# Optimization experiments

Measured on AMD Instinct MI355X. Metric: run time of the kernel, lower is better.

The kernel has to match this reference:

```python
import jax, jax.numpy as jnp
import numpy as np
from jax import lax

BN_EPS = 1e-5
EYE_EPS = 1e-6
ZIP = 128
TAU = 0.2

def _cov(x):
    # x: [C, N] rows=variables, cols=observations (torch.cov semantics)
    n = x.shape[1]
    xc = x - jnp.mean(x, axis=1, keepdims=True)
    return (xc @ xc.T) / (n - 1)

def setup_inputs() -> dict:
    key = jax.random.key(0)
    ks = jax.random.split(key, 10)
    d = {}
    d["img_feats_f"] = jax.random.normal(ks[0], (1, 128, 480, 640), dtype=jnp.float32)
    d["pcd_feats_f"] = jax.random.normal(ks[1], (22432, 128), dtype=jnp.float32)
    # ConvBlock(128->128, k=3, s=1, p=1) + BatchNorm (eval) + ReLU
    d["conv_w"] = jax.random.normal(ks[2], (128, 128, 3, 3), dtype=jnp.float32) * 0.02
    d["conv_b"] = jnp.zeros((128,), dtype=jnp.float32)
    d["bn_gamma"] = jnp.ones((128,), dtype=jnp.float32)
    d["bn_beta"] = jnp.zeros((128,), dtype=jnp.float32)
    d["bn_mean"] = jnp.zeros((128,), dtype=jnp.float32)
    d["bn_var"] = jnp.ones((128,), dtype=jnp.float32)
    # Linear(128->128) + ReLU
    d["lin_w"] = jax.random.normal(ks[3], (128, 128), dtype=jnp.float32) * 0.02
    d["lin_b"] = jnp.zeros((128,), dtype=jnp.float32)
    return d

def reference(img_feats_f, pcd_feats_f, conv_w, conv_b, bn_gamma, bn_beta, bn_mean, bn_var, lin_w, lin_b):
    B, C, h, w = img_feats_f.shape
    # zip_fea_2d: Conv2d(3x3, pad 1) + BN(eval) + ReLU
    x = lax.conv_general_dilated(img_feats_f, conv_w, (1, 1), ((1, 1), (1, 1)),
                                 dimension_numbers=("NCHW", "OIHW", "NCHW"))
    x = x + conv_b[None, :, None, None]
    x = (x - bn_mean[None, :, None, None]) * (bn_gamma / jnp.sqrt(bn_var + BN_EPS))[None, :, None, None] + bn_beta[None, :, None, None]
    img_zip = jax.nn.relu(x)
    # zip_fea_3d: Linear + ReLU
    pcd_zip = jax.nn.relu(pcd_feats_f @ lin_w.T + lin_b)

    tmp_img_f = img_zip.reshape(ZIP, -1)        # [128, h*w]
    tmp_pcd_f = pcd_zip.T                        # [128, Np]
    cov_img = _cov(tmp_img_f)                    # [128, 128]
    cov_pcd = _cov(tmp_pcd_f)                    # [128, 128]

    eye = jnp.eye(ZIP, dtype=cov_img.dtype) * EYE_EPS
    sc_ip = (cov_img @ jnp.linalg.inv(cov_pcd + eye)) / ZIP
    sc_pi = (cov_pcd @ jnp.linalg.inv(cov_img + eye)) / ZIP
    at_ip = jax.nn.softmax(sc_pi, axis=-1)
    at_pi = jax.nn.softmax(sc_ip, axis=-1)
    tmp_img_fb = (at_ip @ tmp_img_f).reshape(-1, h, w)[None]   # [1,128,h,w]
    tmp_pcd_fb = (at_pi @ tmp_pcd_f).T                          # [Np,128]

    at_ii = jax.nn.softmax((cov_img @ cov_img.T) / ZIP, axis=-1)
    at_pp = jax.nn.softmax((cov_pcd @ cov_pcd.T) / ZIP, axis=-1)
    tmp_img_fa = (at_ii @ tmp_img_f).reshape(-1, h, w)[None]
    tmp_pcd_fa = (at_pp @ tmp_pcd_f).T

    img_out = (tmp_img_fb + tmp_img_fa) / 2 * TAU + img_feats_f * (1 - TAU)
    pcd_out = (tmp_pcd_fb + tmp_pcd_fa) / 2 * TAU + pcd_feats_f * (1 - TAU)
    return (img_out, pcd_out)
```

## Files before the change

kernel.cpp:

```cpp
#include <hip/hip_runtime.h>
#include <math.h>

#define HH 480
#define WW 640
#define HWSZ (HH*WW)
#define NPC 22432
#define IMG_SZ (128*HWSZ)
#define NBI 256
#define NBP 64
#define CHUNK_I 1200
#define CHUNK_P 351

typedef unsigned short u16;
typedef unsigned int u32;
typedef __attribute__((ext_vector_type(8))) short bf16x8;
typedef __attribute__((ext_vector_type(4))) float f32x4;

#define OFF_SUMS_IMG 0
#define OFF_SUMS_PCD 128
#define OFF_BIAS2    256
#define OFF_COV_IMG  512
#define OFF_COV_PCD  16896
#define OFF_INV_IMG  33280
#define OFF_INV_PCD  49664
#define OFF_MT_IMG   66048
#define OFF_MT_PCD   82432
#define OFF_LWT      98816
#define OFF_PSUMS    115200
#define OFF_MB       147968
#define OFF_WT       152064
#define OFF_PSUMS_P  OFF_WT
#define OFF_PART_IMG 299520
#define OFF_PART_PCD 4493824
#define OFF_WB       5542400
#define OFF_TIMG_F   5616128
#define TIMG_PAD_W 642
#define TIMG_PX (482*642)
#define TIMG_PLANE (TIMG_PX*32)
#define WS_NEED_FLOATS 25420544
#define OFF_XB       25420544
#define WS_NEED2_FLOATS 45081344

__device__ inline u32 pack_bf16(float a, float b) {
  u32 ua = __float_as_uint(a), ub = __float_as_uint(b);
  ua += 0x7FFFu + ((ua >> 16) & 1u);
  ub += 0x7FFFu + ((ub >> 16) & 1u);
  return (ua >> 16) | (ub & 0xFFFF0000u);
}
__device__ inline u16 to_bf16(float v) {
  u32 u = __float_as_uint(v); u += 0x7FFFu + ((u >> 16) & 1u);
  return (u16)(u >> 16);
}
__device__ inline float from_bf16(u16 v) {
  return __uint_as_float(((u32)v) << 16);
}
__device__ inline float4 f4_fnma(float4 v, float f, float4 p) {
  return make_float4(v.x - f*p.x, v.y - f*p.y, v.z - f*p.z, v.w - f*p.w);
}
__device__ inline void gload_lds16(const void* g, void* l) {
  __builtin_amdgcn_global_load_lds(
      (const __attribute__((address_space(1))) void*)(g),
      (__attribute__((address_space(3))) void*)(l), 16, 0, 0);
}

__global__ void prep_kernel(const float* __restrict__ conv_w, const float* __restrict__ conv_b,
                            const float* __restrict__ gamma, const float* __restrict__ beta,
                            const float* __restrict__ mean, const float* __restrict__ var,
                            const float* __restrict__ lin_w, float* __restrict__ ws, int big) {
  int tid = blockIdx.x * blockDim.x + threadIdx.x;
  int nth = gridDim.x * blockDim.x;
  for (int oc = tid; oc < 128; oc += nth) {
    float s = gamma[oc] / sqrtf(var[oc] + 1e-5f);
    ws[OFF_BIAS2 + oc] = (conv_b[oc] - mean[oc]) * s + beta[oc];
  }
  if (big) {
    u16* Wf = (u16*)(ws + OFF_WB);
    for (int e = tid; e < 9*128*128; e += nth) {
      int j = e & 7, l = (e >> 3) & 63, ob = (e >> 9) & 7;
      int ci32 = (e >> 12) & 3, tap = e >> 14;
      int oc = ob*16 + (l & 15);
      int ci = ci32*32 + ((l >> 4) & 3)*8 + j;
      float s = gamma[oc] / sqrtf(var[oc] + 1e-5f);
      Wf[e] = to_bf16(conv_w[(oc*128 + ci)*9 + tap] * s);
    }
  } else {
    for (int e = tid; e < 128*9*128; e += nth) {
      int oc = e & 127; int k = (e >> 7) % 9; int ci = e / 1152;
      float s = gamma[oc] / sqrtf(var[oc] + 1e-5f);
      ws[OFF_WT + e] = conv_w[(oc*128 + ci)*9 + k] * s;
    }
  }
  for (int e = tid; e < 128*128; e += nth) {
    int c2 = e & 127; int k = e >> 7;
    ws[OFF_LWT + e] = lin_w[c2*128 + k];
  }
}

__launch_bounds__(256)
__global__ void timg_kernel(const float* __restrict__ img, u16* __restrict__ Timg) {
  __shared__ float xt[64][133];
  const int b = blockIdx.x;
  const int t = threadIdx.x;
  if (b >= 4800) {
    int tid = (b - 4800) * 256 + t;
    if (tid < (642*2 + 480*2) * 16) {
      int px = tid >> 4, u = tid & 15;
      int q = u >> 2, j = u & 3;
      int addr;
      if (px < 642) addr = px;
      else if (px < 1284) addr = 481*642 + (px - 642);
      else if (px < 1764) addr = (px - 1284 + 1) * 642;
      else addr = (px - 1764 + 1) * 642 + 641;
      ((uint4*)Timg)[(size_t)q*(TIMG_PX*4) + (size_t)addr*4 + j] = make_uint4(0u,0u,0u,0u);
    }
    return;
  }
  const int h = b / 10, w0 = (b % 10) * 64;
  const int wq = t & 15, cg = t >> 4;
#pragma unroll
  for (int i = 0; i < 8; ++i) {
    int ci = cg + i*16;
    float4 v = *(const float4*)&img[(size_t)ci*HWSZ + h*WW + w0 + wq*4];
    xt[wq*4+0][ci] = v.x; xt[wq*4+1][ci] = v.y;
    xt[wq*4+2][ci] = v.z; xt[wq*4+3][ci] = v.w;
  }
  __syncthreads();
  const int wp = t >> 2, q = t & 3, c0 = q * 32;
  u32 out[16];
#pragma unroll
  for (int j = 0; j < 16; ++j) {
    float a = xt[wp][c0 + 2*j], bb = xt[wp][c0 + 2*j + 1];
    out[j] = pack_bf16(a, bb);
  }
  uint4 ud[4];
#pragma unroll
  for (int u = 0; u < 4; ++u)
    ud[u] = make_uint4(out[u*4], out[u*4+1], out[u*4+2], out[u*4+3]);
  u16* dst = Timg + (size_t)q*TIMG_PLANE
           + ((size_t)(h+1)*TIMG_PAD_W + (w0 + 1 + wp)) * 32;
  const int key = (1 + wp) & 3;
  uint4* d4 = (uint4*)dst;
  switch (key) {
    case 0: d4[0]=ud[0]; d4[1]=ud[1]; d4[2]=ud[2]; d4[3]=ud[3]; break;
    case 1: d4[0]=ud[1]; d4[1]=ud[0]; d4[2]=ud[3]; d4[3]=ud[2]; break;
    case 2: d4[0]=ud[2]; d4[1]=ud[3]; d4[2]=ud[0]; d4[3]=ud[1]; break;
    default: d4[0]=ud[3]; d4[1]=ud[2]; d4[2]=ud[1]; d4[3]=ud[0]; break;
  }
}

#define REG_ROWS 6
#define REG_COLS 66
#define REG_PX (REG_ROWS*REG_COLS)
#define STAGE_E (REG_PX*4)
__launch_bounds__(256, 2)
__global__ void conv_mfma7_kernel(const u16* __restrict__ Timg,
                                  const u16* __restrict__ Wf,
                                  const float* __restrict__ ws,
                                  float* __restrict__ X,
                                  u16* __restrict__ xb) {
  __shared__ __align__(16) u16 reg_lds[1792 * 8];
  const int b = blockIdx.x;
  const int h0 = (b / 10) * 4;
  const int w0 = (b % 10) * 64;
  const int t = threadIdx.x;
  const int wv = t >> 6, l = t & 63;
  const int n_lane = l & 15, k_lane = l >> 4;
  const int ocg = wv & 1;
  const int rowg = wv >> 1;

  f32x4 acc[4][8];
#pragma unroll
  for (int mt = 0; mt < 4; ++mt)
#pragma unroll
    for (int nt = 0; nt < 8; ++nt) acc[mt][nt] = (f32x4){0.f,0.f,0.f,0.f};

#pragma unroll 1
  for (int qc = 0; qc < 4; ++qc) {
    __syncthreads();
    const u16* plane = Timg + (size_t)qc * TIMG_PLANE;
#pragma unroll
    for (int i = 0; i < 7; ++i) {
      int e = t + i*256;
      int ec = (e < STAGE_E) ? e : (STAGE_E - 1);
      int px = ec >> 2, j = ec & 3;
      int r = px / REG_COLS, c = px - r * REG_COLS;
      const u16* src = plane + ((size_t)(h0 + r) * TIMG_PAD_W + (w0 + c)) * 32 + j*8;
      gload_lds16(src, reg_lds + (size_t)e * 8);
    }
    __syncthreads();
    const u16* wq = Wf + (qc*8 + ocg*4)*512 + l*8;
#pragma unroll 1
    for (int tap = 0; tap < 9; ++tap) {
      const int kh = (tap * 11) >> 5;
      const int kw = tap - kh * 3;
      const int cb = n_lane + kw;
      const int rb = rowg*2 + kh;
      const int uoff = (k_lane ^ (cb & 3)) << 4;
      const u16* wtap = wq + tap * 16384;
      bf16x8 Af[4], Bf[8];
#pragma unroll
      for (int mt = 0; mt < 4; ++mt)
        Af[mt] = *(const bf16x8*)(wtap + mt*512);
#pragma unroll
      for (int nt = 0; nt < 8; ++nt) {
        int px = (rb + (nt >> 2)) * REG_COLS + cb + (nt & 3) * 16;
        Bf[nt] = *(const bf16x8*)((char*)reg_lds + px * 64 + uoff);
      }
#pragma unroll
      for (int mt = 0; mt < 4; ++mt)
#pragma unroll
        for (int nt = 0; nt < 8; ++nt)
          acc[mt][nt] = __builtin_amdgcn_mfma_f32_16x16x32_bf16(Af[mt], Bf[nt], acc[mt][nt], 0, 0, 0);
    }
  }
  const float* bias = ws + OFF_BIAS2;
  if (xb) {
#pragma unroll
    for (int mt = 0; mt < 4; ++mt) {
      f32x4 bv = *(const f32x4*)(bias + ocg*64 + mt*16 + k_lane*4);
#pragma unroll
      for (int nt = 0; nt < 8; ++nt) {
        int row = h0 + rowg*2 + (nt >> 2);
        int col = w0 + (nt & 3)*16 + n_lane;
#pragma unroll
        for (int rr = 0; rr < 4; ++rr) {
          int oc = ocg*64 + mt*16 + k_lane*4 + rr;
          float v = acc[mt][nt][rr] + bv[rr];
          xb[(size_t)oc * HWSZ + row*WW + col] = to_bf16(fmaxf(v, 0.f));
        }
      }
    }
  } else {
#pragma unroll
    for (int mt = 0; mt < 4; ++mt) {
      f32x4 bv = *(const f32x4*)(bias + ocg*64 + mt*16 + k_lane*4);
#pragma unroll
      for (int nt = 0; nt < 8; ++nt) {
        int row = h0 + rowg*2 + (nt >> 2);
        int col = w0 + (nt & 3)*16 + n_lane;
#pragma unroll
        for (int rr = 0; rr < 4; ++rr) {
          int oc = ocg*64 + mt*16 + k_lane*4 + rr;
          float v = acc[mt][nt][rr] + bv[rr];
          X[(size_t)oc * HWSZ + row*WW + col] = fmaxf(v, 0.f);
        }
      }
    }
  }
}

__launch_bounds__(256)
__global__ void conv_kernel(const float* __restrict__ img,
                            const float* __restrict__ ws,
                            float* __restrict__ outX) {
  __shared__ __align__(16) float xs[8][10][20];
  __shared__ __align__(16) float wsm[8][9][64];
  const int b = blockIdx.x;
  const int oc0 = (b & 1) * 64;
  const int sidx = b >> 1;
  const int h0 = (sidx / 40) * 8;
  const int w0 = (sidx % 40) * 16;
  const int t = threadIdx.x;
  const int oc_t = t & 15;
  const int px_t = t >> 4;
  const int ph = px_t >> 1;
  const int pw0 = (px_t & 1) * 8;
  float acc[4][8];
#pragma unroll
  for (int o = 0; o < 4; o++)
#pragma unroll
    for (int m = 0; m < 8; m++) acc[o][m] = 0.f;
  const float* wT = ws + OFF_WT;
  for (int ci0 = 0; ci0 < 128; ci0 += 8) {
    __syncthreads();
    for (int e = t; e < 1440; e += 256) {
      int ci = e / 180; int rem = e - ci*180; int r = rem / 18; int cc2 = rem - r*18;
      int gh = h0 + r - 1, gw = w0 + cc2 - 1;
      float v = 0.f;
      if ((unsigned)gh < (unsigned)HH && (unsigned)gw < (unsigned)WW)
        v = img[(ci0+ci)*HWSZ + gh*WW + gw];
      xs[ci][r][cc2] = v;
    }
    for (int e = t; e < 4608; e += 256) {
      int oc = e & 63; int k = (e >> 6) % 9; int ci = e / 576;
      wsm[ci][k][oc] = wT[((ci0+ci)*9 + k)*128 + oc0 + oc];
    }
    __syncthreads();
#pragma unroll
    for (int ci = 0; ci < 8; ci++) {
#pragma unroll
      for (int kh = 0; kh < 3; kh++) {
        float x10[10];
        float4 xa = *(const float4*)&xs[ci][ph+kh][pw0];
        float4 xb2 = *(const float4*)&xs[ci][ph+kh][pw0+4];
        x10[0]=xa.x; x10[1]=xa.y; x10[2]=xa.z; x10[3]=xa.w;
        x10[4]=xb2.x; x10[5]=xb2.y; x10[6]=xb2.z; x10[7]=xb2.w;
        x10[8]=xs[ci][ph+kh][pw0+8]; x10[9]=xs[ci][ph+kh][pw0+9];
#pragma unroll
        for (int kw = 0; kw < 3; kw++) {
          float4 wv = *(const float4*)&wsm[ci][kh*3+kw][oc_t*4];
#pragma unroll
          for (int m = 0; m < 8; m++) {
            float xv = x10[kw+m];
            acc[0][m] += wv.x*xv; acc[1][m] += wv.y*xv;
            acc[2][m] += wv.z*xv; acc[3][m] += wv.w*xv;
          }
        }
      }
    }
  }
#pragma unroll
  for (int o = 0; o < 4; o++) {
    int oc = oc0 + oc_t*4 + o;
    float bias = ws[OFF_BIAS2 + oc];
    float4 r0, r1;
    r0.x = fmaxf(acc[o][0]+bias, 0.f); r0.y = fmaxf(acc[o][1]+bias, 0.f);
    r0.z = fmaxf(acc[o][2]+bias, 0.f); r0.w = fmaxf(acc[o][3]+bias, 0.f);
    r1.x = fmaxf(acc[o][4]+bias, 0.f); r1.y = fmaxf(acc[o][5]+bias, 0.f);
    r1.z = fmaxf(acc[o][6]+bias, 0.f); r1.w = fmaxf(acc[o][7]+bias, 0.f);
    float* dst = outX + (size_t)oc*HWSZ + (h0+ph)*WW + w0 + pw0;
    *(float4*)dst = r0; *(float4*)(dst+4) = r1;
  }
}

__launch_bounds__(256)
__global__ void linear_kernel(const float* __restrict__ pcd,
                              const float* __restrict__ ws,
                              const float* __restrict__ lin_b,
                              float* __restrict__ Z) {
  __shared__ __align__(16) float Mt[128][132];
  __shared__ __align__(16) float zs[16][132];
  const int b = blockIdx.x, t = threadIdx.x;
  const int n0 = b * 16;
#pragma unroll
  for (int i = 0; i < 16; i++) {
    int idx = t + i*256; int r = idx >> 5; int c4 = (idx & 31)*4;
    *(float4*)&Mt[r][c4] = *(const float4*)&ws[OFF_LWT + r*128 + c4];
  }
#pragma unroll
  for (int i = 0; i < 2; i++) {
    int idx = t + i*256; int r = idx >> 5; int c4 = (idx & 31)*4;
    *(float4*)&zs[r][c4] = *(const float4*)&pcd[(size_t)(n0+r)*128 + c4];
  }
  __syncthreads();
  const int nl = t & 15;
  const int c0 = (t >> 4) * 8;
  float acc[8];
#pragma unroll
  for (int q = 0; q < 8; q++) acc[q] = 0.f;
#pragma unroll 8
  for (int k = 0; k < 128; k++) {
    float z = zs[nl][k];
    float4 wa = *(const float4*)&Mt[k][c0];
    float4 wb = *(const float4*)&Mt[k][c0+4];
    acc[0]+=z*wa.x; acc[1]+=z*wa.y; acc[2]+=z*wa.z; acc[3]+=z*wa.w;
    acc[4]+=z*wb.x; acc[5]+=z*wb.y; acc[6]+=z*wb.z; acc[7]+=z*wb.w;
  }
  float4 ba = *(const float4*)&lin_b[c0];
  float4 bb = *(const float4*)&lin_b[c0+4];
  float4 r0, r1;
  r0.x = fmaxf(acc[0]+ba.x,0.f); r0.y = fmaxf(acc[1]+ba.y,0.f);
  r0.z = fmaxf(acc[2]+ba.z,0.f); r0.w = fmaxf(acc[3]+ba.w,0.f);
  r1.x = fmaxf(acc[4]+bb.x,0.f); r1.y = fmaxf(acc[5]+bb.y,0.f);
  r1.z = fmaxf(acc[6]+bb.z,0.f); r1.w = fmaxf(acc[7]+bb.w,0.f);
  float* dst = Z + (size_t)(n0+nl)*128 + c0;
  *(float4*)dst = r0; *(float4*)(dst+4) = r1;
}

__launch_bounds__(256)
__global__ void gram_img_mfma_kernel(const float* __restrict__ X,
                                     const u16* __restrict__ xb,
                                     float* __restrict__ part,
                                     float* __restrict__ psums) {
  __shared__ __align__(16) u16 tile[128*64];
  const int b = blockIdx.x, t = threadIdx.x;
  const int px0 = b * CHUNK_I;
  const int wv = t >> 6, l = t & 63;
  const int i0 = (wv >> 1) * 64, j0 = (wv & 1) * 64;
  const int row16 = l & 15, kq = l >> 4;
  const int pg = t & 15;
  const int g0 = t >> 4;
  const int cb16 = t >> 1, hb16 = t & 1;
  float csum[8];
#pragma unroll
  for (int q = 0; q < 8; ++q) csum[q] = 0.f;
  f32x4 acc[4][4];
#pragma unroll
  for (int a = 0; a < 4; ++a)
#pragma unroll
    for (int q = 0; q < 4; ++q) acc[a][q] = (f32x4){0.f,0.f,0.f,0.f};

  for (int ti = 0; ti < 19; ++ti) {
    if (xb) {
      uint4 v[4];
#pragma unroll
      for (int gi = 0; gi < 4; ++gi) {
        int g = hb16*4 + gi;
        int plg = ti*64 + g*8;
        if (plg < CHUNK_I)
          v[gi] = *(const uint4*)(xb + (size_t)cb16*HWSZ + px0 + plg);
        else
          v[gi] = make_uint4(0u,0u,0u,0u);
      }
      __syncthreads();
#pragma unroll
      for (int gi = 0; gi < 4; ++gi) {
        int g = hb16*4 + gi;
        *(uint4*)((char*)tile + cb16*128 + ((g*16) ^ ((cb16 & 7) << 4))) = v[gi];
        const u16* p16 = (const u16*)&v[gi];
#pragma unroll
        for (int j = 0; j < 8; ++j) csum[0] += from_bf16(p16[j]);
      }
    } else {
      const int plg = ti*64 + pg*4;
      float4 v[8];
      if (ti < 18) {
#pragma unroll
        for (int cc = 0; cc < 8; ++cc) {
          int c = g0 + cc*16;
          v[cc] = *(const float4*)(X + (size_t)c*HWSZ + px0 + plg);
        }
      } else {
#pragma unroll
        for (int cc = 0; cc < 8; ++cc) {
          int c = g0 + cc*16;
          const float* src = X + (size_t)c*HWSZ + px0;
#pragma unroll
          for (int j = 0; j < 4; ++j) {
            int p = plg + j;
            ((float*)&v[cc])[j] = (p < CHUNK_I) ? src[p] : 0.f;
          }
        }
      }
      __syncthreads();
#pragma unroll
      for (int cc = 0; cc < 8; ++cc) {
        int c = g0 + cc*16;
        csum[cc] += v[cc].x + v[cc].y + v[cc].z + v[cc].w;
        u32 w0 = pack_bf16(v[cc].x, v[cc].y);
        u32 w1 = pack_bf16(v[cc].z, v[cc].w);
        *(uint2*)((char*)tile + c*128 + ((pg*8) ^ ((c & 7) << 4))) = make_uint2(w0, w1);
      }
    }
    __syncthreads();
#pragma unroll
    for (int f = 0; f < 2; ++f) {
      bf16x8 Af[4], Bf[4];
#pragma unroll
      for (int mt = 0; mt < 4; ++mt) {
        int c = i0 + mt*16 + row16;
        Af[mt] = *(const bf16x8*)((char*)tile + c*128 + ((f*64 + kq*16) ^ ((c & 7) << 4)));
      }
#pragma unroll
      for (int nt = 0; nt < 4; ++nt) {
        int c = j0 + nt*16 + row16;
        Bf[nt] = *(const bf16x8*)((char*)tile + c*128 + ((f*64 + kq*16) ^ ((c & 7) << 4)));
      }
#pragma unroll
      for (int mt = 0; mt < 4; ++mt)
#pragma unroll
        for (int nt = 0; nt < 4; ++nt)
          acc[mt][nt] = __builtin_amdgcn_mfma_f32_16x16x32_bf16(Af[mt], Bf[nt], acc[mt][nt], 0, 0, 0);
    }
    __syncthreads();
  }
  if (xb) {
    float s = csum[0];
    s += __shfl_xor(s, 1, 64);
    if ((t & 1) == 0) psums[b*128 + cb16] = s;
  } else {
#pragma unroll
    for (int cc = 0; cc < 8; ++cc) {
      float s = csum[cc];
      s += __shfl_xor(s, 1, 64);
      s += __shfl_xor(s, 2, 64);
      s += __shfl_xor(s, 4, 64);
      s += __shfl_xor(s, 8, 64);
      if (pg == 0) psums[b*128 + g0 + cc*16] = s;
    }
  }
  float* dst = part + (size_t)b*16384;
#pragma unroll
  for (int mt = 0; mt < 4; ++mt)
#pragma unroll
    for (int nt = 0; nt < 4; ++nt) {
#pragma unroll
      for (int r = 0; r < 4; ++r) {
        int i = i0 + mt*16 + kq*4 + r;
        int j = j0 + nt*16 + row16;
        dst[i*128 + j] = acc[mt][nt][r];
      }
    }
}

__launch_bounds__(256)
__global__ void gram_pcd_kernel(const float* __restrict__ Z, float* __restrict__ part,
                                float* __restrict__ psums_p) {
  __shared__ __align__(16) float zt[64][132];
  __shared__ float ps4[4][32][4];
  const int b = blockIdx.x, t = threadIdx.x;
  const int n0 = b * CHUNK_P;
  const int i0 = (t >> 4) * 8, j0 = (t & 15) * 8;
  float acc[8][8];
#pragma unroll
  for (int a = 0; a < 8; a++)
#pragma unroll
    for (int q = 0; q < 8; q++) acc[a][q] = 0.f;
  float fsum[4] = {0.f, 0.f, 0.f, 0.f};
  for (int tile = 0; tile < 6; tile++) {
    __syncthreads();
#pragma unroll
    for (int i = 0; i < 8; i++) {
      int idx = t + i*256; int r = idx >> 5; int c4 = (idx & 31)*4;
      int lrow = tile*64 + r;
      int n = n0 + lrow;
      float4 v = {0.f,0.f,0.f,0.f};
      if (lrow < CHUNK_P && n < NPC) v = *(const float4*)&Z[(size_t)n*128 + c4];
      *(float4*)&zt[r][c4] = v;
      fsum[0] += v.x; fsum[1] += v.y; fsum[2] += v.z; fsum[3] += v.w;
    }
    __syncthreads();
#pragma unroll 4
    for (int n = 0; n < 64; n++) {
      float4 a0 = *(const float4*)&zt[n][i0];
      float4 a1 = *(const float4*)&zt[n][i0+4];
      float4 b0 = *(const float4*)&zt[n][j0];
      float4 b1 = *(const float4*)&zt[n][j0+4];
      float av[8] = {a0.x,a0.y,a0.z,a0.w,a1.x,a1.y,a1.z,a1.w};
      float bv[8] = {b0.x,b0.y,b0.z,b0.w,b1.x,b1.y,b1.z,b1.w};
#pragma unroll
      for (int a = 0; a < 8; a++)
#pragma unroll
        for (int q = 0; q < 8; q++) acc[a][q] += av[a]*bv[q];
    }
  }
  float* dst = part + (size_t)b*16384;
#pragma unroll
  for (int a = 0; a < 8; a++) {
    float4 w0v = {acc[a][0],acc[a][1],acc[a][2],acc[a][3]};
    float4 w1v = {acc[a][4],acc[a][5],acc[a][6],acc[a][7]};
    *(float4*)&dst[(i0+a)*128 + j0] = w0v;
    *(float4*)&dst[(i0+a)*128 + j0 + 4] = w1v;
  }
  const int wv2 = t >> 6;
#pragma unroll
  for (int j2 = 0; j2 < 4; ++j2) fsum[j2] += __shfl_down(fsum[j2], 32, 64);
  if ((t & 63) < 32) {
#pragma unroll
    for (int j2 = 0; j2 < 4; ++j2) ps4[wv2][t & 31][j2] = fsum[j2];
  }
  __syncthreads();
  if (t < 128) {
    float s = ps4[0][t>>2][t&3] + ps4[1][t>>2][t&3]
            + ps4[2][t>>2][t&3] + ps4[3][t>>2][t&3];
    psums_p[b*128 + t] = s;
  }
}

__launch_bounds__(128)
__global__ void reduce_cov_kernel(float* __restrict__ ws) {
  const int b = blockIdx.x, t = threadIdx.x;
  const bool isimg = (b < 128);
  const int i = isimg ? b : b - 128;
  const int nparts = isimg ? NBI : NBP;
  const float* part = ws + (isimg ? OFF_PART_IMG : OFF_PART_PCD);
  __shared__ float sums[128];
  if (isimg) {
    const float* ps = ws + OFF_PSUMS;
    float s = 0.f;
    for (int p = 0; p < NBI; ++p) s += ps[p*128 + t];
    sums[t] = s;
  } else {
    const float* psp = ws + OFF_PSUMS_P;
    float s = 0.f;
    for (int p = 0; p < NBP; ++p) s += psp[p*128 + t];
    sums[t] = s;
  }
  __syncthreads();
  float g = 0.f;
  for (int p = 0; p < nparts; p++) g += part[(size_t)p*16384 + i*128 + t];
  float Si = sums[i];
  float Sj = sums[t];
  float n = isimg ? (float)HWSZ : (float)NPC;
  float cov = (g - Si*Sj/n) / (n - 1.f);
  ws[(isimg ? OFF_COV_IMG : OFF_COV_PCD) + i*128 + t] = cov;
}

__launch_bounds__(256, 1)
__global__ void invert_kernel(float* __restrict__ ws) {
  __shared__ float A_[128*132];
  __shared__ float Rb_[16*132];
  __shared__ float prw[16];
  __shared__ float pcl[16];
  const int blk = blockIdx.x, t = threadIdx.x;
  const float* src = ws + (blk == 0 ? OFF_COV_IMG : OFF_COV_PCD);
  float* dst = ws + (blk == 0 ? OFF_INV_IMG : OFF_INV_PCD);
  for (int e = t; e < 16384; e += 256) {
    int i = e >> 7, j = e & 127;
    A_[i*132 + j] = src[e] + ((i == j) ? 1e-6f : 0.f);
  }
#pragma unroll 1
  for (int p = 0; p < 8; ++p) {
    const int k0 = p * 16;
    __syncthreads();
    if (t < 64) {
      const int r = t & 15, cg = t >> 4, cb = cg * 4;
      float4 d = *(const float4*)&A_[(k0 + r)*132 + k0 + cb];
#pragma unroll 1
      for (int k = 0; k < 16; ++k) {
        const int kg = k >> 2, km = k & 3;
        if (r == k) {
          prw[cb+0] = d.x; prw[cb+1] = d.y; prw[cb+2] = d.z; prw[cb+3] = d.w;
        }
        if (cg == kg) {
          float el = (km==0) ? d.x : (km==1) ? d.y : (km==2) ? d.z : d.w;
          pcl[r] = el;
        }
        __builtin_amdgcn_wave_barrier();
        float ip = 1.f / pcl[k];
        float f  = pcl[r];
        float p0 = prw[cb+0], p1 = prw[cb+1], p2 = prw[cb+2], p3 = prw[cb+3];
        __builtin_amdgcn_wave_barrier();
        if (r == k) {
          d.x *= ip; d.y *= ip; d.z *= ip; d.w *= ip;
          if (cg == kg) { if (km==0) d.x=ip; else if (km==1) d.y=ip; else if (km==2) d.z=ip; else d.w=ip; }
        } else {
          float g = f * ip;
          d.x -= g*p0; d.y -= g*p1; d.z -= g*p2; d.w -= g*p3;
          if (cg == kg) { if (km==0) d.x=-g; else if (km==1) d.y=-g; else if (km==2) d.z=-g; else d.w=-g; }
        }
        __builtin_amdgcn_wave_barrier();
      }
      *(float4*)&Rb_[r*132 + k0 + cb] = d;
    }
    __syncthreads();
    {
      const int r = t & 15, ch = t >> 4;
      if ((ch >> 1) != p) {
        const int j0 = ch * 8;
        float4 dv0 = *(const float4*)&Rb_[r*132 + k0];
        float4 dv1 = *(const float4*)&Rb_[r*132 + k0 + 4];
        float4 dv2 = *(const float4*)&Rb_[r*132 + k0 + 8];
        float4 dv3 = *(const float4*)&Rb_[r*132 + k0 + 12];
        float dv[16] = {dv0.x,dv0.y,dv0.z,dv0.w, dv1.x,dv1.y,dv1.z,dv1.w,
                        dv2.x,dv2.y,dv2.z,dv2.w, dv3.x,dv3.y,dv3.z,dv3.w};
        float4 a0 = {0,0,0,0}, a1 = {0,0,0,0};
#pragma unroll
        for (int s = 0; s < 16; ++s) {
          float4 r0v = *(const float4*)&A_[(k0+s)*132 + j0];
          float4 r1v = *(const float4*)&A_[(k0+s)*132 + j0 + 4];
          float w = dv[s];
          a0.x += w*r0v.x; a0.y += w*r0v.y; a0.z += w*r0v.z; a0.w += w*r0v.w;
          a1.x += w*r1v.x; a1.y += w*r1v.y; a1.z += w*r1v.z; a1.w += w*r1v.w;
        }
        *(float4*)&Rb_[r*132 + j0] = a0;
        *(float4*)&Rb_[r*132 + j0 + 4] = a1;
      }
    }
    __syncthreads();
    {
      const int tr = t >> 4, tc = t & 15;
      const int r0 = tr * 8, c0 = tc * 8;
      const bool pivrow = (tr >> 1) == p;
      const bool pivcol = (tc >> 1) == p;
      float4 acc[8][2];
      float4 F4[8][4];
      if (pivrow) {
#pragma unroll
        for (int i = 0; i < 8; ++i) {
          acc[i][0] = *(const float4*)&Rb_[(r0 + i - k0)*132 + c0];
          acc[i][1] = *(const float4*)&Rb_[(r0 + i - k0)*132 + c0 + 4];
        }
      } else {
#pragma unroll
        for (int i = 0; i < 8; ++i) {
          F4[i][0] = *(const float4*)&A_[(r0+i)*132 + k0];
          F4[i][1] = *(const float4*)&A_[(r0+i)*132 + k0 + 4];
          F4[i][2] = *(const float4*)&A_[(r0+i)*132 + k0 + 8];
          F4[i][3] = *(const float4*)&A_[(r0+i)*132 + k0 + 12];
        }
        if (pivcol) {
#pragma unroll
          for (int i = 0; i < 8; ++i) {
            acc[i][0] = make_float4(0.f,0.f,0.f,0.f);
            acc[i][1] = make_float4(0.f,0.f,0.f,0.f);
          }
        } else {
#pragma unroll
          for (int i = 0; i < 8; ++i) {
            acc[i][0] = *(const float4*)&A_[(r0+i)*132 + c0];
            acc[i][1] = *(const float4*)&A_[(r0+i)*132 + c0 + 4];
          }
        }
      }
      __syncthreads();
      if (!pivrow) {
#pragma unroll
        for (int s = 0; s < 16; ++s) {
          float4 rb0 = *(const float4*)&Rb_[s*132 + c0];
          float4 rb1 = *(const float4*)&Rb_[s*132 + c0 + 4];
#pragma unroll
          for (int i = 0; i < 8; ++i) {
            float fs = (s&3)==0 ? F4[i][s>>2].x : (s&3)==1 ? F4[i][s>>2].y
                     : (s&3)==2 ? F4[i][s>>2].z : F4[i][s>>2].w;
            acc[i][0] = f4_fnma(acc[i][0], fs, rb0);
            acc[i][1] = f4_fnma(acc[i][1], fs, rb1);
          }
        }
      }
#pragma unroll
      for (int i = 0; i < 8; ++i) {
        *(float4*)&A_[(r0+i)*132 + c0]     = acc[i][0];
        *(float4*)&A_[(r0+i)*132 + c0 + 4] = acc[i][1];
      }
    }
  }
  __syncthreads();
  for (int e = t; e < 16384; e += 256)
    dst[e] = A_[(e >> 7)*132 + (e & 127)];
}

__launch_bounds__(128)
__global__ void attn_kernel(float* __restrict__ ws) {
  const int b = blockIdx.x, j = threadIdx.x;
  const bool isimg = (b < 128);
  const int i = isimg ? b : b - 128;
  const float* rowA = ws + (isimg ? OFF_COV_PCD : OFF_COV_IMG) + i*128;
  const float* matA = ws + (isimg ? OFF_INV_IMG : OFF_INV_PCD);
  const float* rowB = ws + (isimg ? OFF_COV_IMG : OFF_COV_PCD) + i*128;
  const float* matB = ws + (isimg ? OFF_COV_IMG : OFF_COV_PCD);
  __shared__ float rA[128], rB[128], red[128];
  rA[j] = rowA[j]; rB[j] = rowB[j];
  __syncthreads();
  float dA = 0.f, dB = 0.f;
#pragma unroll 8
  for (int k = 0; k < 128; ++k) {
    dA += rA[k] * matA[k*128 + j];
    dB += rB[k] * matB[k*128 + j];
  }
  dA *= 0.0078125f; dB *= 0.0078125f;
  red[j] = dA; __syncthreads();
  for (int s2 = 64; s2 > 0; s2 >>= 1) { if (j < s2) red[j] = fmaxf(red[j], red[j+s2]); __syncthreads(); }
  float mA = red[0]; __syncthreads();
  float eA = expf(dA - mA);
  red[j] = eA; __syncthreads();
  for (int s2 = 64; s2 > 0; s2 >>= 1) { if (j < s2) red[j] += red[j+s2]; __syncthreads(); }
  float sA = red[0]; __syncthreads();
  red[j] = dB; __syncthreads();
  for (int s2 = 64; s2 > 0; s2 >>= 1) { if (j < s2) red[j] = fmaxf(red[j], red[j+s2]); __syncthreads(); }
  float mB = red[0]; __syncthreads();
  float eB = expf(dB - mB);
  red[j] = eB; __syncthreads();
  for (int s2 = 64; s2 > 0; s2 >>= 1) { if (j < s2) red[j] += red[j+s2]; __syncthreads(); }
  float sB = red[0]; __syncthreads();
  float m = 0.1f * (eA/sA + eB/sB);
  if (isimg) {
    int f = j >> 5, ob = i >> 4, l = ((j >> 3) & 3)*16 + (i & 15), jj = j & 7;
    ((u16*)(ws + OFF_MB))[(f*8 + ob)*512 + l*8 + jj] = to_bf16(m);
  } else {
    ws[OFF_MT_PCD + j*128 + i] = m;
  }
}

__launch_bounds__(256, 4)
__global__ void img_final_mfma_kernel(const float* __restrict__ img_in,
                                      const float* __restrict__ ws,
                                      const u16* __restrict__ xb,
                                      float* __restrict__ io) {
  __shared__ __align__(16) char smem[34816];
  u16* bt = (u16*)smem;
  float* ts = (float*)smem;
  const int blk = blockIdx.x, t = threadIdx.x;
  const int px0 = blk * 128;
  const int pxg = (t & 31) * 4;
  const int cp0 = t >> 5;
  if (xb) {
#pragma unroll
    for (int cc = 0; cc < 8; ++cc) {
      int cpair = cp0 + cc*8;
      const u16* s0 = xb + (size_t)(2*cpair)*HWSZ + px0 + pxg;
      uint2 ua = *(const uint2*)s0;
      uint2 ub = *(const uint2*)(s0 + HWSZ);
      u32 w[4];
      w[0] = (ua.x & 0xFFFFu) | ((ub.x & 0xFFFFu) << 16);
      w[1] = (ua.x >> 16)     | (ub.x & 0xFFFF0000u);
      w[2] = (ua.y & 0xFFFFu) | ((ub.y & 0xFFFFu) << 16);
      w[3] = (ua.y >> 16)     | (ub.y & 0xFFFF0000u);
#pragma unroll
      for (int j = 0; j < 4; ++j) {
        int pxl = pxg + j;
        *(u32*)((char*)bt + pxl*256 + ((cpair*4) ^ ((pxl & 7) << 4))) = w[j];
      }
    }
  } else {
#pragma unroll
    for (int cc = 0; cc < 8; ++cc) {
      int cpair = cp0 + cc*8;
      const float* s0 = io + (size_t)(2*cpair)*HWSZ + px0 + pxg;
      float4 a = *(const float4*)s0;
      float4 b4 = *(const float4*)(s0 + HWSZ);
#pragma unroll
      for (int j = 0; j < 4; ++j) {
        int pxl = pxg + j;
        *(u32*)((char*)bt + pxl*256 + ((cpair*4) ^ ((pxl & 7) << 4))) =
            pack_bf16(((const float*)&a)[j], ((const float*)&b4)[j]);
      }
    }
  }
  __syncthreads();
  const int wv = t >> 6, l = t & 63;
  const int i0 = (wv >> 1) * 64, j0 = (wv & 1) * 64;
  const int row16 = l & 15, kq = l >> 4;
  const u16* Mbf = (const u16*)(ws + OFF_MB);
  f32x4 acc[4][4];
#pragma unroll
  for (int a = 0; a < 4; ++a)
#pragma unroll
    for (int q = 0; q < 4; ++q) acc[a][q] = (f32x4){0.f,0.f,0.f,0.f};
#pragma unroll
  for (int f = 0; f < 4; ++f) {
    bf16x8 Bf[4], Am[4];
#pragma unroll
    for (int nt = 0; nt < 4; ++nt) {
      int pxl = j0 + nt*16 + row16;
      Bf[nt] = *(const bf16x8*)((char*)bt + pxl*256 + ((f*64 + kq*16) ^ ((pxl & 7) << 4)));
    }
#pragma unroll
    for (int mt = 0; mt < 4; ++mt) {
      int ob = (wv >> 1) * 4 + mt;
      Am[mt] = *(const bf16x8*)(Mbf + (f*8 + ob)*512 + l*8);
    }
#pragma unroll
    for (int mt = 0; mt < 4; ++mt)
#pragma unroll
      for (int nt = 0; nt < 4; ++nt)
        acc[mt][nt] = __builtin_amdgcn_mfma_f32_16x16x32_bf16(Am[mt], Bf[nt], acc[mt][nt], 0, 0, 0);
  }
#pragma unroll 1
  for (int half = 0; half < 2; ++half) {
    __syncthreads();
    if ((wv & 1) == half) {
#pragma unroll
      for (int mt = 0; mt < 4; ++mt)
#pragma unroll
        for (int nt = 0; nt < 4; ++nt) {
          int lpx = nt*16 + row16;
#pragma unroll
          for (int r = 0; r < 4; ++r) {
            int c = i0 + mt*16 + kq*4 + r;
            ts[c*68 + lpx] = acc[mt][nt][r];
          }
        }
    }
    __syncthreads();
    const int cq = t >> 2, p4 = (t & 3) * 4;
#pragma unroll
    for (int cp = 0; cp < 2; ++cp) {
      int c = cp*64 + cq;
#pragma unroll
      for (int j = 0; j < 4; ++j) {
        int lpx = p4 + j*16;
        float4 v = *(const float4*)&ts[c*68 + lpx];
        size_t off = (size_t)c*HWSZ + px0 + half*64 + lpx;
        float4 o = *(const float4*)&img_in[off];
        float4 r;
        r.x = v.x + 0.8f*o.x; r.y = v.y + 0.8f*o.y;
        r.z = v.z + 0.8f*o.z; r.w = v.w + 0.8f*o.w;
        *(float4*)&io[off] = r;
      }
    }
  }
}

__launch_bounds__(256)
__global__ void pcd_final_kernel(const float* __restrict__ pcd_in,
                                 const float* __restrict__ ws,
                                 float* __restrict__ Z) {
  __shared__ __align__(16) float Mt[128][132];
  __shared__ __align__(16) float zs[16][132];
  const int b = blockIdx.x, t = threadIdx.x;
  const int n0 = b * 16;
#pragma unroll
  for (int i = 0; i < 16; i++) {
    int idx = t + i*256; int r = idx >> 5; int c4 = (idx & 31)*4;
    *(float4*)&Mt[r][c4] = *(const float4*)&ws[OFF_MT_PCD + r*128 + c4];
  }
#pragma unroll
  for (int i = 0; i < 2; i++) {
    int idx = t + i*256; int r = idx >> 5; int c4 = (idx & 31)*4;
    *(float4*)&zs[r][c4] = *(const float4*)&Z[(size_t)(n0+r)*128 + c4];
  }
  __syncthreads();
  const int nl = t & 15;
  const int c0 = (t >> 4) * 8;
  float acc[8];
#pragma unroll
  for (int q = 0; q < 8; q++) acc[q] = 0.f;
#pragma unroll 8
  for (int k = 0; k < 128; k++) {
    float z = zs[nl][k];
    float4 wa = *(const float4*)&Mt[k][c0];
    float4 wb = *(const float4*)&Mt[k][c0+4];
    acc[0]+=z*wa.x; acc[1]+=z*wa.y; acc[2]+=z*wa.z; acc[3]+=z*wa.w;
    acc[4]+=z*wb.x; acc[5]+=z*wb.y; acc[6]+=z*wb.z; acc[7]+=z*wb.w;
  }
  size_t off = (size_t)(n0+nl)*128 + c0;
  float4 pa = *(const float4*)&pcd_in[off];
  float4 pb = *(const float4*)&pcd_in[off+4];
  float4 r0, r1;
  r0.x = acc[0] + 0.8f*pa.x; r0.y = acc[1] + 0.8f*pa.y;
  r0.z = acc[2] + 0.8f*pa.z; r0.w = acc[3] + 0.8f*pa.w;
  r1.x = acc[4] + 0.8f*pb.x; r1.y = acc[5] + 0.8f*pb.y;
  r1.z = acc[6] + 0.8f*pb.z; r1.w = acc[7] + 0.8f*pb.w;
  *(float4*)&Z[off] = r0; *(float4*)&Z[off+4] = r1;
}

extern "C" void kernel_launch(void* const* d_in, const int* in_sizes, int n_in,
                              void* d_out, int out_size, void* d_ws, size_t ws_size,
                              hipStream_t stream) {
  (void)in_sizes; (void)n_in; (void)out_size;
  const float* img_in = (const float*)d_in[0];
  const float* pcd_in = (const float*)d_in[1];
  const float* conv_w = (const float*)d_in[2];
  const float* conv_b = (const float*)d_in[3];
  const float* gamma  = (const float*)d_in[4];
  const float* beta   = (const float*)d_in[5];
  const float* mean   = (const float*)d_in[6];
  const float* var    = (const float*)d_in[7];
  const float* lin_w  = (const float*)d_in[8];
  const float* lin_b  = (const float*)d_in[9];
  float* out = (float*)d_out;
  float* X = out;
  float* Z = out + IMG_SZ;
  float* ws = (float*)d_ws;
  const int big  = (ws_size >= (size_t)WS_NEED_FLOATS * 4) ? 1 : 0;
  const int big2 = (ws_size >= (size_t)WS_NEED2_FLOATS * 4) ? 1 : 0;
  u16* Xb = big2 ? (u16*)(ws + OFF_XB) : (u16*)nullptr;

  hipLaunchKernelGGL(prep_kernel, dim3(64), dim3(256), 0, stream,
                     conv_w, conv_b, gamma, beta, mean, var, lin_w, ws, big);
  if (big) {
    u16* Timg = (u16*)(ws + OFF_TIMG_F);
    u16* Wf = (u16*)(ws + OFF_WB);
    hipLaunchKernelGGL(timg_kernel, dim3(4941), dim3(256), 0, stream, img_in, Timg);
    hipLaunchKernelGGL(conv_mfma7_kernel, dim3(1200), dim3(256), 0, stream, Timg, Wf, ws, X, Xb);
  } else {
    hipLaunchKernelGGL(conv_kernel, dim3(4800), dim3(256), 0, stream, img_in, ws, X);
  }
  hipLaunchKernelGGL(linear_kernel, dim3(NPC/16), dim3(256), 0, stream, pcd_in, ws, lin_b, Z);
  hipLaunchKernelGGL(gram_img_mfma_kernel, dim3(NBI), dim3(256), 0, stream,
                     X, Xb, ws + OFF_PART_IMG, ws + OFF_PSUMS);
  hipLaunchKernelGGL(gram_pcd_kernel, dim3(NBP), dim3(256), 0, stream,
                     Z, ws + OFF_PART_PCD, ws + OFF_PSUMS_P);
  hipLaunchKernelGGL(reduce_cov_kernel, dim3(256), dim3(128), 0, stream, ws);
  hipLaunchKernelGGL(invert_kernel, dim3(2), dim3(256), 0, stream, ws);
  hipLaunchKernelGGL(attn_kernel, dim3(256), dim3(128), 0, stream, ws);
  hipLaunchKernelGGL(img_final_mfma_kernel, dim3(HWSZ/128), dim3(256), 0, stream,
                     img_in, ws, Xb, X);
  hipLaunchKernelGGL(pcd_final_kernel, dim3(NPC/16), dim3(256), 0, stream, pcd_in, ws, Z);
}
```

Baseline: 534.7 us.

## Double-buffer conv LDS staging, prefetch gram tiles, and change swizzle key

The conv kernel now uses two LDS buffers and issues async global-to-LDS loads for the next channel quarter while MFMAs run on the current one, which removes one barrier per quarter. The gram bf16 path register-prefetches the next tile before the MFMA block. The swizzle key in both the Timg writer and the conv reader moves from bits 0-1 to bits 2-3 of the pixel column, changing the LDS bank-conflict pattern. Doubling LDS per block may hurt the two-blocks-per-CU occupancy target, and the async prefetch relies on the barrier at the end of each iteration for ordering.

```diff
diff --git a/kernel.cpp b/kernel.cpp
--- a/kernel.cpp
+++ b/kernel.cpp
@@ -138,7 +138,7 @@
     ud[u] = make_uint4(out[u*4], out[u*4+1], out[u*4+2], out[u*4+3]);
   u16* dst = Timg + (size_t)q*TIMG_PLANE
            + ((size_t)(h+1)*TIMG_PAD_W + (w0 + 1 + wp)) * 32;
-  const int key = (1 + wp) & 3;
+  const int key = ((1 + wp) >> 2) & 3;
   uint4* d4 = (uint4*)dst;
   switch (key) {
     case 0: d4[0]=ud[0]; d4[1]=ud[1]; d4[2]=ud[2]; d4[3]=ud[3]; break;
@@ -152,13 +152,14 @@
 #define REG_COLS 66
 #define REG_PX (REG_ROWS*REG_COLS)
 #define STAGE_E (REG_PX*4)
+#define BUF_E 1792
 __launch_bounds__(256, 2)
-__global__ void conv_mfma7_kernel(const u16* __restrict__ Timg,
+__global__ void conv_mfma8_kernel(const u16* __restrict__ Timg,
                                   const u16* __restrict__ Wf,
                                   const float* __restrict__ ws,
                                   float* __restrict__ X,
                                   u16* __restrict__ xb) {
-  __shared__ __align__(16) u16 reg_lds[1792 * 8];
+  __shared__ __align__(16) u16 reg_lds[2][BUF_E * 8];
   const int b = blockIdx.x;
   const int h0 = (b / 10) * 4;
   const int w0 = (b % 10) * 64;
@@ -174,10 +175,8 @@
 #pragma unroll
     for (int nt = 0; nt < 8; ++nt) acc[mt][nt] = (f32x4){0.f,0.f,0.f,0.f};
 
-#pragma unroll 1
-  for (int qc = 0; qc < 4; ++qc) {
-    __syncthreads();
-    const u16* plane = Timg + (size_t)qc * TIMG_PLANE;
+  {
+    const u16* plane = Timg;
 #pragma unroll
     for (int i = 0; i < 7; ++i) {
       int e = t + i*256;
@@ -185,9 +184,28 @@
       int px = ec >> 2, j = ec & 3;
       int r = px / REG_COLS, c = px - r * REG_COLS;
       const u16* src = plane + ((size_t)(h0 + r) * TIMG_PAD_W + (w0 + c)) * 32 + j*8;
-      gload_lds16(src, reg_lds + (size_t)e * 8);
-    }
-    __syncthreads();
+      gload_lds16(src, reg_lds[0] + (size_t)e * 8);
+    }
+  }
+  __syncthreads();
+
+  int cur = 0;
+#pragma unroll 1
+  for (int qc = 0; qc < 4; ++qc) {
+    if (qc < 3) {
+      const u16* plane = Timg + (size_t)(qc+1) * TIMG_PLANE;
+      u16* dstb = reg_lds[cur ^ 1];
+#pragma unroll
+      for (int i = 0; i < 7; ++i) {
+        int e = t + i*256;
+        int ec = (e < STAGE_E) ? e : (STAGE_E - 1);
+        int px = ec >> 2, j = ec & 3;
+        int r = px / REG_COLS, c = px - r * REG_COLS;
+        const u16* src = plane + ((size_t)(h0 + r) * TIMG_PAD_W + (w0 + c)) * 32 + j*8;
+        gload_lds16(src, dstb + (size_t)e * 8);
+      }
+    }
+    const u16* curb = reg_lds[cur];
     const u16* wq = Wf + (qc*8 + ocg*4)*512 + l*8;
 #pragma unroll 1
     for (int tap = 0; tap < 9; ++tap) {
@@ -195,7 +213,7 @@
       const int kw = tap - kh * 3;
       const int cb = n_lane + kw;
       const int rb = rowg*2 + kh;
-      const int uoff = (k_lane ^ (cb & 3)) << 4;
+      const int uoff = (k_lane ^ ((cb >> 2) & 3)) << 4;
       const u16* wtap = wq + tap * 16384;
       bf16x8 Af[4], Bf[8];
 #pragma unroll
@@ -204,7 +222,7 @@
 #pragma unroll
       for (int nt = 0; nt < 8; ++nt) {
         int px = (rb + (nt >> 2)) * REG_COLS + cb + (nt & 3) * 16;
-        Bf[nt] = *(const bf16x8*)((char*)reg_lds + px * 64 + uoff);
+        Bf[nt] = *(const bf16x8*)((const char*)curb + px * 64 + uoff);
       }
 #pragma unroll
       for (int mt = 0; mt < 4; ++mt)
@@ -212,6 +230,8 @@
         for (int nt = 0; nt < 8; ++nt)
           acc[mt][nt] = __builtin_amdgcn_mfma_f32_16x16x32_bf16(Af[mt], Bf[nt], acc[mt][nt], 0, 0, 0);
     }
+    __syncthreads();
+    cur ^= 1;
   }
   const float* bias = ws + OFF_BIAS2;
   if (xb) {
@@ -390,28 +410,60 @@
 #pragma unroll
     for (int q = 0; q < 4; ++q) acc[a][q] = (f32x4){0.f,0.f,0.f,0.f};
 
-  for (int ti = 0; ti < 19; ++ti) {
-    if (xb) {
-      uint4 v[4];
+  if (xb) {
+    uint4 vcur[4];
+#pragma unroll
+    for (int gi = 0; gi < 4; ++gi) {
+      int g = hb16*4 + gi;
+      vcur[gi] = *(const uint4*)(xb + (size_t)cb16*HWSZ + px0 + g*8);
+    }
+#pragma unroll 1
+    for (int ti = 0; ti < 19; ++ti) {
+      __syncthreads();
 #pragma unroll
       for (int gi = 0; gi < 4; ++gi) {
         int g = hb16*4 + gi;
-        int plg = ti*64 + g*8;
-        if (plg < CHUNK_I)
-          v[gi] = *(const uint4*)(xb + (size_t)cb16*HWSZ + px0 + plg);
-        else
-          v[gi] = make_uint4(0u,0u,0u,0u);
-      }
-      __syncthreads();
+        *(uint4*)((char*)tile + cb16*128 + ((g*16) ^ ((cb16 & 7) << 4))) = vcur[gi];
+        const u16* p16 = (const u16*)&vcur[gi];
+#pragma unroll
+        for (int j = 0; j < 8; ++j) csum[0] += from_bf16(p16[j]);
+      }
+      uint4 vnext[4];
 #pragma unroll
       for (int gi = 0; gi < 4; ++gi) {
         int g = hb16*4 + gi;
-        *(uint4*)((char*)tile + cb16*128 + ((g*16) ^ ((cb16 & 7) << 4))) = v[gi];
-        const u16* p16 = (const u16*)&v[gi];
-#pragma unroll
-        for (int j = 0; j < 8; ++j) csum[0] += from_bf16(p16[j]);
-      }
-    } else {
+        int plg = (ti+1)*64 + g*8;
+        if (ti < 18 && plg < CHUNK_I)
+          vnext[gi] = *(const uint4*)(xb + (size_t)cb16*HWSZ + px0 + plg);
+        else
+          vnext[gi] = make_uint4(0u,0u,0u,0u);
+      }
+      __syncthreads();
+#pragma unroll
+      for (int f = 0; f < 2; ++f) {
+        bf16x8 Af[4], Bf[4];
+#pragma unroll
+        for (int mt = 0; mt < 4; ++mt) {
+          int c = i0 + mt*16 + row16;
+          Af[mt] = *(const bf16x8*)((char*)tile + c*128 + ((f*64 + kq*16) ^ ((c & 7) << 4)));
+        }
+#pragma unroll
+        for (int nt = 0; nt < 4; ++nt) {
+          int c = j0 + nt*16 + row16;
+          Bf[nt] = *(const bf16x8*)((char*)tile + c*128 + ((f*64 + kq*16) ^ ((c & 7) << 4)));
+        }
+#pragma unroll
+        for (int mt = 0; mt < 4; ++mt)
+#pragma unroll
+          for (int nt = 0; nt < 4; ++nt)
+            acc[mt][nt] = __builtin_amdgcn_mfma_f32_16x16x32_bf16(Af[mt], Bf[nt], acc[mt][nt], 0, 0, 0);
+      }
+#pragma unroll
+      for (int gi = 0; gi < 4; ++gi) vcur[gi] = vnext[gi];
+    }
+  } else {
+#pragma unroll 1
+    for (int ti = 0; ti < 19; ++ti) {
       const int plg = ti*64 + pg*4;
       float4 v[8];
       if (ti < 18) {
@@ -441,28 +493,28 @@
         u32 w1 = pack_bf16(v[cc].z, v[cc].w);
         *(uint2*)((char*)tile + c*128 + ((pg*8) ^ ((c & 7) << 4))) = make_uint2(w0, w1);
       }
-    }
-    __syncthreads();
-#pragma unroll
-    for (int f = 0; f < 2; ++f) {
-      bf16x8 Af[4], Bf[4];
-#pragma unroll
-      for (int mt = 0; mt < 4; ++mt) {
-        int c = i0 + mt*16 + row16;
-        Af[mt] = *(const bf16x8*)((char*)tile + c*128 + ((f*64 + kq*16) ^ ((c & 7) << 4)));
-      }
-#pragma unroll
-      for (int nt = 0; nt < 4; ++nt) {
-        int c = j0 + nt*16 + row16;
-        Bf[nt] = *(const bf16x8*)((char*)tile + c*128 + ((f*64 + kq*16) ^ ((c & 7) << 4)));
-      }
-#pragma unroll
-      for (int mt = 0; mt < 4; ++mt)
-#pragma unroll
-        for (int nt = 0; nt < 4; ++nt)
-          acc[mt][nt] = __builtin_amdgcn_mfma_f32_16x16x32_bf16(Af[mt], Bf[nt], acc[mt][nt], 0, 0, 0);
-    }
-    __syncthreads();
+      __syncthreads();
+#pragma unroll
+      for (int f = 0; f < 2; ++f) {
+        bf16x8 Af[4], Bf[4];
+#pragma unroll
+        for (int mt = 0; mt < 4; ++mt) {
+          int c = i0 + mt*16 + row16;
+          Af[mt] = *(const bf16x8*)((char*)tile + c*128 + ((f*64 + kq*16) ^ ((c & 7) << 4)));
+        }
+#pragma unroll
+        for (int nt = 0; nt < 4; ++nt) {
+          int c = j0 + nt*16 + row16;
+          Bf[nt] = *(const bf16x8*)((char*)tile + c*128 + ((f*64 + kq*16) ^ ((c & 7) << 4)));
+        }
+#pragma unroll
+        for (int mt = 0; mt < 4; ++mt)
+#pragma unroll
+          for (int nt = 0; nt < 4; ++nt)
+            acc[mt][nt] = __builtin_amdgcn_mfma_f32_16x16x32_bf16(Af[mt], Bf[nt], acc[mt][nt], 0, 0, 0);
+      }
+      __syncthreads();
+    }
   }
   if (xb) {
     float s = csum[0];
@@ -943,7 +995,7 @@
     u16* Timg = (u16*)(ws + OFF_TIMG_F);
     u16* Wf = (u16*)(ws + OFF_WB);
     hipLaunchKernelGGL(timg_kernel, dim3(4941), dim3(256), 0, stream, img_in, Timg);
-    hipLaunchKernelGGL(conv_mfma7_kernel, dim3(1200), dim3(256), 0, stream, Timg, Wf, ws, X, Xb);
+    hipLaunchKernelGGL(conv_mfma8_kernel, dim3(1200), dim3(256), 0, stream, Timg, Wf, ws, X, Xb);
   } else {
     hipLaunchKernelGGL(conv_kernel, dim3(4800), dim3(256), 0, stream, img_in, ws, X);
   }
```

Measured after the change: 531.1 us (median of 2 runs). About the same (-0.7%).
